# Kernel optimization log

Hardware: AMD Instinct MI355X
Metric: run time of the kernel (lower is better)

Reference implementation:

```python
import jax, jax.numpy as jnp
import numpy as np

B, S, D = 32, 512, 512
H, DH = 8, 64          # head_num, att_embedding_size
DFF = 4 * D
NEG = float(-2**32 + 1)
LN_EPS = 1e-3          # keras LayerNormalization default


def layer_norm(x, gamma, beta):
    mu = jnp.mean(x, axis=-1, keepdims=True)
    var = jnp.mean(jnp.square(x - mu), axis=-1, keepdims=True)
    return (x - mu) / jnp.sqrt(var + LN_EPS) * gamma + beta


def setup_inputs() -> dict:
    key = jax.random.key(0)
    ks = jax.random.split(key, 10)
    queries = jax.random.normal(ks[0], (B, S, D), dtype=jnp.float32)
    keys = jax.random.normal(ks[1], (B, S, D), dtype=jnp.float32)
    query_lens = jax.random.randint(ks[2], (B, 1), 1, S + 1)
    key_lens = jax.random.randint(ks[3], (B, 1), 1, S + 1)
    # learned params (TruncatedNormal stddev 0.05-ish / Glorot approximated by scaled normals)
    W_Q = jax.random.normal(ks[4], (D, D), dtype=jnp.float32) * 0.05
    W_K = jax.random.normal(ks[5], (D, D), dtype=jnp.float32) * 0.05
    W_V = jax.random.normal(ks[6], (D, D), dtype=jnp.float32) * 0.05
    fw1 = jax.random.normal(ks[7], (D, DFF), dtype=jnp.float32) * (1.0 / np.sqrt(D))
    fw2 = jax.random.normal(ks[8], (DFF, D), dtype=jnp.float32) * (1.0 / np.sqrt(DFF))
    ln_gamma = jnp.ones((D,), dtype=jnp.float32)
    ln_beta = jnp.zeros((D,), dtype=jnp.float32)
    return {"queries": queries, "keys": keys, "W_Q": W_Q, "W_K": W_K, "W_V": W_V,
            "fw1": fw1, "fw2": fw2, "ln_gamma": ln_gamma, "ln_beta": ln_beta,
            "query_lens": query_lens, "key_lens": key_lens}


def reference(queries, keys, W_Q, W_K, W_V, fw1, fw2, ln_gamma, ln_beta, query_lens, key_lens):
    # masks from sequence lengths: [B, S] float {0,1}
    pos = jnp.arange(S)
    q_mask = (pos[None, :] < query_lens).astype(queries.dtype)  # [B,S]
    k_mask = (pos[None, :] < key_lens).astype(queries.dtype)    # [B,S]

    # QKV projections, split into heads: [B,S,H,DH]
    Q = (queries @ W_Q).reshape(B, S, H, DH)
    Kp = (keys @ W_K).reshape(B, S, H, DH)
    V = (keys @ W_V).reshape(B, S, H, DH)

    # scaled dot-product scores: [B,H,Sq,Sk]
    scores = jnp.einsum('bqhd,bkhd->bhqk', Q, Kp) / jnp.sqrt(jnp.asarray(DH, queries.dtype))

    # key padding mask
    scores = jnp.where(k_mask[:, None, None, :] == 1, scores, NEG)
    # blinding: kill the diagonal (self-position)
    eye = jnp.eye(S, dtype=bool)
    scores = jnp.where(eye[None, None, :, :], NEG, scores)

    scores = scores - jnp.max(scores, axis=-1, keepdims=True)
    attn = jax.nn.softmax(scores, axis=-1)
    # query mask zeros out padded query rows (after softmax, as in source)
    attn = attn * q_mask[:, None, :, None]

    out = jnp.einsum('bhqk,bkhd->bqhd', attn, V).reshape(B, S, D)

    result = out + queries                       # use_res
    result = layer_norm(result, ln_gamma, ln_beta)  # shared ln (use_layer_norm)

    # feed-forward
    h = jax.nn.relu(result @ fw1) @ fw2
    result = result + h
    result = layer_norm(result, ln_gamma, ln_beta)

    # output_type == 'mean'
    return jnp.mean(result, axis=1, keepdims=True)  # [B,1,D]
```

## Files before the change

kernel.cpp:

```cpp
#include <hip/hip_runtime.h>

typedef unsigned short ushort_t;
typedef unsigned int uint_t;
typedef __attribute__((ext_vector_type(4))) float f32x4;
typedef __attribute__((ext_vector_type(2))) float f32x2;
typedef __attribute__((ext_vector_type(8))) short s16x8;
typedef __attribute__((ext_vector_type(8))) _Float16 f16x8;
typedef __attribute__((ext_vector_type(4))) unsigned short u16x4;

#define NEGV -60000.0f

__device__ __forceinline__ ushort_t f2bf(float f) {
  unsigned int u = __builtin_bit_cast(unsigned int, f);
  return (ushort_t)((u + 0x7fffu + ((u >> 16) & 1u)) >> 16);
}
__device__ __forceinline__ float bf2f(ushort_t h) {
  unsigned int u = ((unsigned int)h) << 16;
  return __builtin_bit_cast(float, u);
}
__device__ __forceinline__ void gload_lds16(const void* g, void* l) {
  __builtin_amdgcn_global_load_lds(
      (const __attribute__((address_space(1))) unsigned int*)g,
      (__attribute__((address_space(3))) unsigned int*)l, 16, 0, 0);
}

template<int EPI>
__global__ __launch_bounds__(256)
void gemm_bt(const ushort_t* __restrict__ A, const ushort_t* __restrict__ A2,
             int lda,
             const ushort_t* __restrict__ Bt, int ldb,
             void* __restrict__ Cv, int ldc, int K,
             long long sB, long long sC)
{
  __shared__ ushort_t As[2][128 * 32];
  __shared__ ushort_t Bs[2][128 * 32];

  const int tid = threadIdx.x;
  const int w = tid >> 6;
  const int lane = tid & 63;
  const int z = blockIdx.z;

  const ushort_t* Az = (z == 0) ? A : A2;
  const ushort_t* Bz = Bt + (size_t)z * sB;

  const int orig = blockIdx.x + gridDim.x * blockIdx.y;
  const int bx = (orig >> 3) % gridDim.x;
  const int by = (orig & 7) + 8 * ((orig >> 3) / gridDim.x);
  const int m0 = by * 128;
  const int n0 = bx * 128;

  const int wm = (w >> 1) * 64;
  const int wn = (w & 1) * 64;

  f32x4 acc[4][4];
#pragma unroll
  for (int m = 0; m < 4; ++m)
#pragma unroll
    for (int n = 0; n < 4; ++n)
      acc[m][n] = (f32x4){0.f, 0.f, 0.f, 0.f};

  const int cA0 = w * 64 + lane;
  const int cA1 = 256 + cA0;
  const int rA0 = cA0 >> 2, kO0 = (cA0 & 3) * 8;
  const int rA1 = cA1 >> 2, kO1 = (cA1 & 3) * 8;

  auto stage = [&](int p, int k0) {
    gload_lds16(Az + (size_t)(m0 + rA0) * lda + (k0 + kO0),
                As[p] + (size_t)(w * 64) * 8);
    gload_lds16(Az + (size_t)(m0 + rA1) * lda + (k0 + kO1),
                As[p] + (size_t)(256 + w * 64) * 8);
    gload_lds16(Bz + (size_t)(n0 + rA0) * ldb + (k0 + kO0),
                Bs[p] + (size_t)(w * 64) * 8);
    gload_lds16(Bz + (size_t)(n0 + rA1) * ldb + (k0 + kO1),
                Bs[p] + (size_t)(256 + w * 64) * 8);
  };

  const int nk = K >> 5;
  stage(0, 0);
  __syncthreads();
  for (int kt = 0; kt < nk; ++kt) {
    const int p = kt & 1;
    if (kt + 1 < nk) stage(p ^ 1, (kt + 1) << 5);

    s16x8 af[4], bfr[4];
#pragma unroll
    for (int m = 0; m < 4; ++m)
      af[m] = *(const s16x8*)(As[p] + (size_t)(wm + m * 16 + (lane & 15)) * 32 +
                              ((lane >> 4) * 8));
#pragma unroll
    for (int n = 0; n < 4; ++n)
      bfr[n] = *(const s16x8*)(Bs[p] + (size_t)(wn + n * 16 + (lane & 15)) * 32 +
                               ((lane >> 4) * 8));
#pragma unroll
    for (int m = 0; m < 4; ++m)
#pragma unroll
      for (int n = 0; n < 4; ++n)
        acc[m][n] = __builtin_amdgcn_mfma_f32_16x16x32_bf16(af[m], bfr[n],
                                                            acc[m][n], 0, 0, 0);
    __syncthreads();
  }

  const float s0 = (EPI == 4 && z == 0) ? 0.125f : 1.0f;
  char* Cz = (char*)Cv + (size_t)sC * z;
  const int r_base = (lane >> 4) * 4;
  const int c_base = lane & 15;
#pragma unroll
  for (int m = 0; m < 4; ++m)
#pragma unroll
    for (int n = 0; n < 4; ++n)
#pragma unroll
      for (int j = 0; j < 4; ++j) {
        const int rg = m0 + wm + m * 16 + r_base + j;
        const int cg = n0 + wn + n * 16 + c_base;
        float v = acc[m][n][j];
        const size_t idx = (size_t)rg * ldc + cg;
        if constexpr (EPI == 0) {
          ((float*)Cz)[idx] = v;
        } else if constexpr (EPI == 2) {
          ((ushort_t*)Cz)[idx] = f2bf(fmaxf(v, 0.f));
        } else {
          ((ushort_t*)Cz)[idx] = f2bf(v * s0);
        }
      }
}

__global__ __launch_bounds__(256, 4)
void flash_attn(const ushort_t* __restrict__ Qg, const ushort_t* __restrict__ Kg,
                const ushort_t* __restrict__ Vt, ushort_t* __restrict__ AOb,
                const int* __restrict__ qlen, const int* __restrict__ klen)
{
  __shared__ ushort_t sm[20480];
  ushort_t* PQ = sm + 16384;

  const int tid = threadIdx.x, w = tid >> 6, lane = tid & 63;
  const int fr = lane & 15, fq = lane >> 4;

  int id = blockIdx.x;
  id = (id & 7) * 256 + (id >> 3);
  const int qt = id & 7, h = (id >> 3) & 7, b = id >> 6;
  const int q0 = qt * 64;
  const int KL = klen[b], QL = qlen[b];

  if (q0 >= QL) {
#pragma unroll
    for (int i = 0; i < 4; ++i) {
      int idx = i * 256 + tid;
      int rr = idx >> 4, cc = (idx & 15) << 2;
      *(u16x4*)&AOb[((size_t)(b * 512 + q0 + rr)) * 512 + h * 64 + cc] =
          (u16x4){0, 0, 0, 0};
    }
    return;
  }

  int nt = (KL + 63) >> 6;
  if (KL == 1) nt = 8;

  const ushort_t* Qrow = Qg + ((size_t)(b * 512 + q0)) * 512 + h * 64;
  const ushort_t* Krow = Kg + ((size_t)b * 512) * 512 + h * 64;
  const ushort_t* Vrow = Vt + (((size_t)b * 8 + h) * 64) * 512;

#pragma unroll
  for (int i = 0; i < 2; ++i) {
    int s = i * 256 + tid, r = s >> 3, c = (s & 7) ^ (r & 7);
    gload_lds16(Qrow + (size_t)r * 512 + c * 8, PQ + (i * 256 + w * 64) * 8);
  }
#pragma unroll
  for (int i = 0; i < 2; ++i) {
    int s = i * 256 + tid, r = s >> 3, c = (s & 7) ^ (r & 7);
    gload_lds16(Krow + (size_t)r * 512 + c * 8, sm + (i * 256 + w * 64) * 8);
    gload_lds16(Vrow + (size_t)r * 512 + c * 8, sm + 4096 + (i * 256 + w * 64) * 8);
  }
  __syncthreads();

  s16x8 qf[2];
#pragma unroll
  for (int kc = 0; kc < 2; ++kc) {
    int r = w * 16 + fr;
    qf[kc] = *(const s16x8*)(PQ + r * 64 + (((kc * 4 + fq) ^ (r & 7)) * 8));
  }

  float mrun[4], lrun[4];
  f32x4 oacc[4];
#pragma unroll
  for (int j = 0; j < 4; ++j) { mrun[j] = -1e30f; lrun[j] = 0.f; }
#pragma unroll
  for (int nd = 0; nd < 4; ++nd) oacc[nd] = (f32x4){0.f, 0.f, 0.f, 0.f};

  for (int t = 0; t < nt; ++t) {
    ushort_t* Kb = sm + (t & 1) * 8192;
    ushort_t* Vb = Kb + 4096;
    if (t + 1 < nt) {
      const int kv1 = (t + 1) * 64;
      ushort_t* Kn = sm + ((t + 1) & 1) * 8192;
#pragma unroll
      for (int i = 0; i < 2; ++i) {
        int s = i * 256 + tid, r = s >> 3, c = (s & 7) ^ (r & 7);
        gload_lds16(Krow + (size_t)(kv1 + r) * 512 + c * 8,
                    Kn + (i * 256 + w * 64) * 8);
        gload_lds16(Vrow + (size_t)r * 512 + kv1 + c * 8,
                    Kn + 4096 + (i * 256 + w * 64) * 8);
      }
    }
    const int kv0 = t * 64;

    f32x4 sacc[4];
#pragma unroll
    for (int n = 0; n < 4; ++n) sacc[n] = (f32x4){0.f, 0.f, 0.f, 0.f};
#pragma unroll
    for (int n = 0; n < 4; ++n)
#pragma unroll
      for (int kc = 0; kc < 2; ++kc) {
        int r = n * 16 + fr;
        s16x8 kf = *(const s16x8*)(Kb + r * 64 + (((kc * 4 + fq) ^ (r & 7)) * 8));
        sacc[n] = __builtin_amdgcn_mfma_f32_16x16x32_bf16(qf[kc], kf, sacc[n], 0, 0, 0);
      }

#pragma unroll
    for (int j = 0; j < 4; ++j) {
      const int rl = w * 16 + fq * 4 + j;
      const int rg = q0 + rl;
      float sv[4];
      float tmax = -1e30f;
#pragma unroll
      for (int n = 0; n < 4; ++n) {
        int cg = kv0 + n * 16 + fr;
        float v = sacc[n][j];
        if (cg >= KL || cg == rg) v = NEGV;
        sv[n] = v;
        tmax = fmaxf(tmax, v);
      }
#pragma unroll
      for (int o = 1; o < 16; o <<= 1) tmax = fmaxf(tmax, __shfl_xor(tmax, o));
      const float mnew = fmaxf(mrun[j], tmax);
      const float sf = __expf(mrun[j] - mnew);
      mrun[j] = mnew;
      float ps = 0.f;
      _Float16* prow = (_Float16*)(PQ + rl * 64);
#pragma unroll
      for (int n = 0; n < 4; ++n) {
        float p = __expf(sv[n] - mnew);
        ps += p;
        int cl = n * 2 + (fr >> 3);
        prow[((cl ^ (rl & 7)) * 8) + (fr & 7)] = (_Float16)p;
      }
      lrun[j] = lrun[j] * sf + ps;
#pragma unroll
      for (int nd = 0; nd < 4; ++nd) oacc[nd][j] *= sf;
    }

#pragma unroll
    for (int kc = 0; kc < 2; ++kc) {
      const int rl = w * 16 + fr;
      s16x8 pf = *(const s16x8*)(PQ + rl * 64 + (((kc * 4 + fq) ^ (rl & 7)) * 8));
#pragma unroll
      for (int nd = 0; nd < 4; ++nd) {
        int d = nd * 16 + fr;
        s16x8 vf = *(const s16x8*)(Vb + d * 64 + (((kc * 4 + fq) ^ (d & 7)) * 8));
        oacc[nd] = __builtin_amdgcn_mfma_f32_16x16x32_f16(
            __builtin_bit_cast(f16x8, pf), __builtin_bit_cast(f16x8, vf),
            oacc[nd], 0, 0, 0);
      }
    }
    __syncthreads();
  }

#pragma unroll
  for (int j = 0; j < 4; ++j) {
    float l = lrun[j];
#pragma unroll
    for (int o = 1; o < 16; o <<= 1) l += __shfl_xor(l, o);
    const int rg = q0 + w * 16 + fq * 4 + j;
    const float inv = (rg < QL) ? (1.f / l) : 0.f;
#pragma unroll
    for (int nd = 0; nd < 4; ++nd)
      AOb[((size_t)(b * 512 + rg)) * 512 + h * 64 + nd * 16 + fr] =
          f2bf(oacc[nd][j] * inv);
  }
}

__global__ __launch_bounds__(256) void cvt_bf16(const float* __restrict__ in,
                                                ushort_t* __restrict__ out, int n4) {
  int i = blockIdx.x * 256 + threadIdx.x;
  if (i >= n4) return;
  f32x4 v = ((const f32x4*)in)[i];
  u16x4 o;
#pragma unroll
  for (int j = 0; j < 4; ++j) o[j] = f2bf(v[j]);
  ((u16x4*)out)[i] = o;
}

__global__ __launch_bounds__(256) void transpose_cvt(const float* __restrict__ in,
                                                     ushort_t* __restrict__ out,
                                                     int R, int C) {
  __shared__ float tile[32][33];
  const int c0 = blockIdx.x * 32, r0 = blockIdx.y * 32;
  const int tx = threadIdx.x & 31, ty = threadIdx.x >> 5;
#pragma unroll
  for (int i = 0; i < 32; i += 8)
    tile[ty + i][tx] = in[(size_t)(r0 + ty + i) * C + (c0 + tx)];
  __syncthreads();
#pragma unroll
  for (int i = 0; i < 32; i += 8)
    out[(size_t)(c0 + ty + i) * R + (r0 + tx)] = f2bf(tile[tx][ty + i]);
}

__global__ __launch_bounds__(256) void build_vt(const ushort_t* __restrict__ V,
                                                ushort_t* __restrict__ Vt) {
  __shared__ ushort_t tile[64 * 65];
  const int s0 = blockIdx.x * 64, h = blockIdx.y, b = blockIdx.z;
  const int t = threadIdx.x;
#pragma unroll
  for (int i = 0; i < 16; ++i) {
    int idx = i * 256 + t;
    int sl = idx >> 6, d = idx & 63;
    tile[sl * 65 + d] = V[(size_t)(b * 512 + s0 + sl) * 512 + h * 64 + d];
  }
  __syncthreads();
  _Float16* vt = (_Float16*)Vt;
#pragma unroll
  for (int i = 0; i < 16; ++i) {
    int idx = i * 256 + t;
    int d = idx >> 6, sl = idx & 63;
    vt[((size_t)(b * 8 + h) * 64 + d) * 512 + (s0 + sl)] =
        (_Float16)bf2f(tile[sl * 65 + d]);
  }
}

__global__ __launch_bounds__(256) void ln1(const ushort_t* __restrict__ xb,
                                           const float* __restrict__ r,
                                           const float* __restrict__ g,
                                           const float* __restrict__ be,
                                           ushort_t* __restrict__ ob) {
  const int row = blockIdx.x, t = threadIdx.x;
  const size_t base = (size_t)row * 512;
  const uint_t xv = ((const uint_t*)(xb + base))[t];
  const f32x2 rv = ((const f32x2*)(r + base))[t];
  float v0 = bf2f((ushort_t)(xv & 0xffff)) + rv[0];
  float v1 = bf2f((ushort_t)(xv >> 16)) + rv[1];
  float s = v0 + v1, q = v0 * v0 + v1 * v1;
#pragma unroll
  for (int o = 32; o; o >>= 1) { s += __shfl_xor(s, o); q += __shfl_xor(q, o); }
  __shared__ float ps[4], pq[4];
  const int w = t >> 6, lane = t & 63;
  if (lane == 0) { ps[w] = s; pq[w] = q; }
  __syncthreads();
  s = ps[0] + ps[1] + ps[2] + ps[3];
  q = pq[0] + pq[1] + pq[2] + pq[3];
  const float mu = s * 0.001953125f;
  const float var = q * 0.001953125f - mu * mu;
  const float inv = 1.0f / sqrtf(var + 1e-3f);
  const float y0 = (v0 - mu) * inv * g[2 * t] + be[2 * t];
  const float y1 = (v1 - mu) * inv * g[2 * t + 1] + be[2 * t + 1];
  ((uint_t*)(ob + base))[t] = (uint_t)f2bf(y0) | ((uint_t)f2bf(y1) << 16);
}

__global__ __launch_bounds__(256) void ln2(const float* __restrict__ h2a,
                                           const float* __restrict__ h2b,
                                           const ushort_t* __restrict__ r1b,
                                           const float* __restrict__ g,
                                           const float* __restrict__ be,
                                           ushort_t* __restrict__ ob) {
  const int row = blockIdx.x, t = threadIdx.x;
  const size_t base = (size_t)row * 512;
  const f32x2 a = ((const f32x2*)(h2a + base))[t];
  const f32x2 b = ((const f32x2*)(h2b + base))[t];
  const uint_t rv = ((const uint_t*)(r1b + base))[t];
  float v0 = a[0] + b[0] + bf2f((ushort_t)(rv & 0xffff));
  float v1 = a[1] + b[1] + bf2f((ushort_t)(rv >> 16));
  float s = v0 + v1, q = v0 * v0 + v1 * v1;
#pragma unroll
  for (int o = 32; o; o >>= 1) { s += __shfl_xor(s, o); q += __shfl_xor(q, o); }
  __shared__ float ps[4], pq[4];
  const int w = t >> 6, lane = t & 63;
  if (lane == 0) { ps[w] = s; pq[w] = q; }
  __syncthreads();
  s = ps[0] + ps[1] + ps[2] + ps[3];
  q = pq[0] + pq[1] + pq[2] + pq[3];
  const float mu = s * 0.001953125f;
  const float var = q * 0.001953125f - mu * mu;
  const float inv = 1.0f / sqrtf(var + 1e-3f);
  const float y0 = (v0 - mu) * inv * g[2 * t] + be[2 * t];
  const float y1 = (v1 - mu) * inv * g[2 * t + 1] + be[2 * t + 1];
  ((uint_t*)(ob + base))[t] = (uint_t)f2bf(y0) | ((uint_t)f2bf(y1) << 16);
}

__global__ void mean_partial(const ushort_t* __restrict__ r3,
                             float* __restrict__ part) {
  const int sc = blockIdx.x, b = blockIdx.y, d = threadIdx.x;
  float s = 0.f;
#pragma unroll 4
  for (int i = 0; i < 64; ++i)
    s += bf2f(r3[(size_t)(b * 512 + sc * 64 + i) * 512 + d]);
  part[(size_t)(b * 8 + sc) * 512 + d] = s;
}
__global__ void mean_final(const float* __restrict__ part, float* __restrict__ out) {
  const int b = blockIdx.x, d = threadIdx.x;
  float s = 0.f;
#pragma unroll
  for (int i = 0; i < 8; ++i) s += part[(size_t)(b * 8 + i) * 512 + d];
  out[b * 512 + d] = s * (1.0f / 512.0f);
}

extern "C" void kernel_launch(void* const* d_in, const int* in_sizes, int n_in,
                              void* d_out, int out_size, void* d_ws, size_t ws_size,
                              hipStream_t stream) {
  (void)in_sizes; (void)n_in; (void)out_size; (void)ws_size;
  const float* queries = (const float*)d_in[0];
  const float* keys    = (const float*)d_in[1];
  const float* W_Q = (const float*)d_in[2];
  const float* W_K = (const float*)d_in[3];
  const float* W_V = (const float*)d_in[4];
  const float* fw1 = (const float*)d_in[5];
  const float* fw2 = (const float*)d_in[6];
  const float* ln_g = (const float*)d_in[7];
  const float* ln_b = (const float*)d_in[8];
  const int* qlen = (const int*)d_in[9];
  const int* klen = (const int*)d_in[10];
  float* out = (float*)d_out;

  char* ws = (char*)d_ws;
  const size_t MB = 1048576;
  ushort_t* XQ  = (ushort_t*)(ws + 0 * MB);
  ushort_t* XK  = (ushort_t*)(ws + 16 * MB);
  ushort_t* Qb  = (ushort_t*)(ws + 32 * MB);
  ushort_t* Vb  = (ushort_t*)(ws + 64 * MB);
  ushort_t* VT  = (ushort_t*)(ws + 80 * MB);
  ushort_t* AOb = (ushort_t*)(ws + 96 * MB);
  ushort_t* R1B = (ushort_t*)(ws + 112 * MB);
  ushort_t* H1  = (ushort_t*)(ws + 0 * MB);
  float*    H2  = (float*)(ws + 128 * MB);
  ushort_t* R3B = (ushort_t*)(ws + 192 * MB);
  char*     wsw = ws + 208 * MB;
  ushort_t* WQT  = (ushort_t*)(wsw);
  ushort_t* FW1T = (ushort_t*)(wsw + 3 * 524288);
  ushort_t* FW2T = (ushort_t*)(wsw + 3 * 524288 + 2097152);
  float*    PART = (float*)(wsw + 3 * 524288 + 2 * 2097152);

  cvt_bf16<<<8192, 256, 0, stream>>>(queries, XQ, 2097152);
  cvt_bf16<<<8192, 256, 0, stream>>>(keys, XK, 2097152);
  transpose_cvt<<<dim3(16, 16), 256, 0, stream>>>(W_Q, WQT, 512, 512);
  transpose_cvt<<<dim3(16, 16), 256, 0, stream>>>(W_K, WQT + 262144, 512, 512);
  transpose_cvt<<<dim3(16, 16), 256, 0, stream>>>(W_V, WQT + 524288, 512, 512);
  transpose_cvt<<<dim3(64, 16), 256, 0, stream>>>(fw1, FW1T, 512, 2048);
  transpose_cvt<<<dim3(16, 64), 256, 0, stream>>>(fw2, FW2T, 2048, 512);
  gemm_bt<4><<<dim3(4, 128, 3), 256, 0, stream>>>(
      XQ, XK, 512, WQT, 512, (void*)Qb, 512, 512, 262144, 16 * MB);
  build_vt<<<dim3(8, 8, 32), 256, 0, stream>>>(Vb, VT);
  flash_attn<<<2048, 256, 0, stream>>>(Qb, Qb + 8388608, VT, AOb, qlen, klen);
  ln1<<<16384, 256, 0, stream>>>(AOb, queries, ln_g, ln_b, R1B);
  gemm_bt<2><<<dim3(16, 128, 1), 256, 0, stream>>>(
      R1B, R1B, 512, FW1T, 512, (void*)H1, 2048, 512, 0, 0);
  gemm_bt<0><<<dim3(4, 128, 2), 256, 0, stream>>>(
      H1, H1 + 1024, 2048, FW2T, 2048, (void*)H2, 512, 1024, 1024, 32 * MB);
  ln2<<<16384, 256, 0, stream>>>(H2, H2 + 8388608, R1B, ln_g, ln_b, R3B);
  mean_partial<<<dim3(8, 32), 512, 0, stream>>>(R3B, PART);
  mean_final<<<32, 512, 0, stream>>>(PART, out);
}
```

Measured before the change: 249.5 us.

## Triple-buffer GEMM LDS staging with swizzled layout and explicit vmcnt waits

The bf16 GEMM moves from double to triple buffering of the A/B LDS tiles. Loads are issued two k-steps ahead and waited on with explicit s_waitcnt vmcnt counts plus raw barriers instead of __syncthreads. The k-offset within each 32-element row is XOR-swizzled by row bits to reduce LDS bank conflicts on the fragment reads, and s_setprio raises wave priority around the MFMA block. This costs 50% more LDS per block, which may reduce occupancy, and relies on exact vmcnt accounting being correct.

```diff
diff --git a/kernel.cpp b/kernel.cpp
--- a/kernel.cpp
+++ b/kernel.cpp
@@ -32,8 +32,8 @@
              void* __restrict__ Cv, int ldc, int K,
              long long sB, long long sC)
 {
-  __shared__ ushort_t As[2][128 * 32];
-  __shared__ ushort_t Bs[2][128 * 32];
+  __shared__ ushort_t As[3][128 * 32];
+  __shared__ ushort_t Bs[3][128 * 32];
 
   const int tid = threadIdx.x;
   const int w = tid >> 6;
@@ -61,8 +61,8 @@
 
   const int cA0 = w * 64 + lane;
   const int cA1 = 256 + cA0;
-  const int rA0 = cA0 >> 2, kO0 = (cA0 & 3) * 8;
-  const int rA1 = cA1 >> 2, kO1 = (cA1 & 3) * 8;
+  const int rA0 = cA0 >> 2, kO0 = (((cA0 & 3) ^ ((rA0 >> 1) & 3)) * 8);
+  const int rA1 = cA1 >> 2, kO1 = (((cA1 & 3) ^ ((rA1 >> 1) & 3)) * 8);
 
   auto stage = [&](int p, int k0) {
     gload_lds16(Az + (size_t)(m0 + rA0) * lda + (k0 + kO0),
@@ -77,27 +77,41 @@
 
   const int nk = K >> 5;
   stage(0, 0);
-  __syncthreads();
+  stage(1, 32);
   for (int kt = 0; kt < nk; ++kt) {
-    const int p = kt & 1;
-    if (kt + 1 < nk) stage(p ^ 1, (kt + 1) << 5);
+    const int p = kt % 3;
+    if (kt + 2 < nk) {
+      stage((kt + 2) % 3, (kt + 2) << 5);
+      asm volatile("s_waitcnt vmcnt(8)" ::: "memory");
+    } else if (kt + 1 < nk) {
+      asm volatile("s_waitcnt vmcnt(4)" ::: "memory");
+    } else {
+      asm volatile("s_waitcnt vmcnt(0)" ::: "memory");
+    }
+    __builtin_amdgcn_s_barrier();
 
     s16x8 af[4], bfr[4];
 #pragma unroll
-    for (int m = 0; m < 4; ++m)
-      af[m] = *(const s16x8*)(As[p] + (size_t)(wm + m * 16 + (lane & 15)) * 32 +
-                              ((lane >> 4) * 8));
-#pragma unroll
-    for (int n = 0; n < 4; ++n)
-      bfr[n] = *(const s16x8*)(Bs[p] + (size_t)(wn + n * 16 + (lane & 15)) * 32 +
-                               ((lane >> 4) * 8));
+    for (int m = 0; m < 4; ++m) {
+      const int r = wm + m * 16 + (lane & 15);
+      af[m] = *(const s16x8*)(As[p] + (size_t)r * 32 +
+                              (((lane >> 4) ^ ((r >> 1) & 3)) * 8));
+    }
+#pragma unroll
+    for (int n = 0; n < 4; ++n) {
+      const int r = wn + n * 16 + (lane & 15);
+      bfr[n] = *(const s16x8*)(Bs[p] + (size_t)r * 32 +
+                               (((lane >> 4) ^ ((r >> 1) & 3)) * 8));
+    }
+    __builtin_amdgcn_s_setprio(1);
 #pragma unroll
     for (int m = 0; m < 4; ++m)
 #pragma unroll
       for (int n = 0; n < 4; ++n)
         acc[m][n] = __builtin_amdgcn_mfma_f32_16x16x32_bf16(af[m], bfr[n],
                                                             acc[m][n], 0, 0, 0);
-    __syncthreads();
+    __builtin_amdgcn_s_setprio(0);
+    __builtin_amdgcn_s_barrier();
   }
 
   const float s0 = (EPI == 4 && z == 0) ? 0.125f : 1.0f;
```

Result: slower. 258.8 us (+3.7%).
